# Performance work log

Hardware: AMD Instinct MI355X
Metric: run time of the kernel (lower is better)

## Reference

```python
import jax, jax.numpy as jnp
import numpy as np

N_GAUSS = 1024
L_FEAT = 8
H_IMG = 128
W_IMG = 128
TANFOVX = 0.7
TANFOVY = 0.7
SCALE_MOD = 1.0


def _quat_to_rot(q):
    # normalized quaternion (r, x, y, z) -> rotation matrix [N,3,3]
    q = q / jnp.linalg.norm(q, axis=-1, keepdims=True)
    r, x, y, z = q[:, 0], q[:, 1], q[:, 2], q[:, 3]
    return jnp.stack([
        1 - 2 * (y * y + z * z), 2 * (x * y - r * z), 2 * (x * z + r * y),
        2 * (x * y + r * z), 1 - 2 * (x * x + z * z), 2 * (y * z - r * x),
        2 * (x * z - r * y), 2 * (y * z + r * x), 1 - 2 * (x * x + y * y)],
        axis=-1).reshape(-1, 3, 3)


def _render(means3D, feats, opac, scales, rots, viewmatrix, projmatrix, bg):
    """EWA-splat rasterization: project, 2D cov, depth sort, front-to-back alpha blend."""
    H, W = H_IMG, W_IMG
    fx = W / (2.0 * TANFOVX)
    fy = H / (2.0 * TANFOVY)
    mh = jnp.concatenate([means3D, jnp.ones_like(means3D[:, :1])], axis=1)  # [N,4]
    t = mh @ viewmatrix            # camera space (row-vector / torch-3DGS convention)
    tz = t[:, 2]
    ph = mh @ projmatrix           # clip space
    pw = 1.0 / (ph[:, 3] + 1e-7)
    pix_x = ((ph[:, 0] * pw + 1.0) * W - 1.0) * 0.5
    pix_y = ((ph[:, 1] * pw + 1.0) * H - 1.0) * 0.5
    # 3D covariance from scale + quaternion
    R = _quat_to_rot(rots)
    M = R * (SCALE_MOD * scales)[:, None, :]
    cov3d = jnp.einsum('nij,nkj->nik', M, M)        # [N,3,3]
    # EWA projection of covariance to 2D
    limx, limy = 1.3 * TANFOVX, 1.3 * TANFOVY
    txz = jnp.clip(t[:, 0] / tz, -limx, limx) * tz
    tyz = jnp.clip(t[:, 1] / tz, -limy, limy) * tz
    zero = jnp.zeros_like(tz)
    J = jnp.stack([
        jnp.stack([fx / tz, zero, -fx * txz / (tz * tz)], axis=-1),
        jnp.stack([zero, fy / tz, -fy * tyz / (tz * tz)], axis=-1)], axis=1)  # [N,2,3]
    Wr = viewmatrix[:3, :3].T
    T2 = jnp.einsum('nij,jk->nik', J, Wr)
    cov2 = jnp.einsum('nij,njk,nlk->nil', T2, cov3d, T2)
    cov2 = cov2 + 0.3 * jnp.eye(2, dtype=cov2.dtype)  # low-pass blur, as in CUDA kernel
    det = cov2[:, 0, 0] * cov2[:, 1, 1] - cov2[:, 0, 1] ** 2
    inv_det = 1.0 / (det + 1e-12)
    ca = cov2[:, 1, 1] * inv_det
    cb = -cov2[:, 0, 1] * inv_det
    cc = cov2[:, 0, 0] * inv_det
    mid = 0.5 * (cov2[:, 0, 0] + cov2[:, 1, 1])
    lam1 = mid + jnp.sqrt(jnp.maximum(0.1, mid * mid - det))
    valid = (tz > 0.2) & (det > 0)
    radii = jnp.where(valid, jnp.ceil(3.0 * jnp.sqrt(lam1)), 0.0).astype(jnp.int32)
    # global front-to-back depth order (equiv. to per-tile depth sort here)
    order = jnp.argsort(jnp.where(valid, tz, jnp.inf))
    tz_s, px_s, py_s = tz[order], pix_x[order], pix_y[order]
    ca_s, cb_s, cc_s = ca[order], cb[order], cc[order]
    op_s, feats_s, valid_s = opac[order, 0], feats[order], valid[order]
    ys, xs = jnp.meshgrid(jnp.arange(H, dtype=tz.dtype), jnp.arange(W, dtype=tz.dtype), indexing='ij')
    pxf, pyf = xs.reshape(-1), ys.reshape(-1)        # [P]
    dx = px_s[None, :] - pxf[:, None]                # [P,N]
    dy = py_s[None, :] - pyf[:, None]
    power = -0.5 * (ca_s * dx * dx + cc_s * dy * dy) - cb_s * dx * dy
    alpha = jnp.minimum(0.99, op_s * jnp.exp(power))
    alpha = jnp.where((power > 0) | (alpha < 1.0 / 255.0) | (~valid_s), 0.0, alpha)
    Tcum = jnp.cumprod(1.0 - alpha, axis=1)
    Tprev = jnp.concatenate([jnp.ones_like(Tcum[:, :1]), Tcum[:, :-1]], axis=1)
    w = alpha * Tprev                                # blending weights [P,N]
    img = jnp.einsum('pn,nc->pc', w, feats_s)
    Tfinal = Tcum[:, -1]
    if bg is not None:
        img = img + Tfinal[:, None] * bg[None, :]
    depth_img = (w @ tz_s).reshape(H, W)
    opacity_img = (1.0 - Tfinal).reshape(H, W)
    n_t = jnp.zeros(alpha.shape[1], jnp.int32).at[order].set(
        jnp.sum(alpha > 0, axis=0).astype(jnp.int32))
    img = img.reshape(H, W, -1).transpose(2, 0, 1)   # [C,H,W]
    return img, radii, depth_img, opacity_img, n_t


def setup_inputs() -> dict:
    key = jax.random.key(0)
    ks = jax.random.split(key, 10)
    N, L = N_GAUSS, L_FEAT
    xy = jax.random.uniform(ks[0], (N, 2), minval=-1.5, maxval=1.5)
    z = jax.random.uniform(ks[1], (N, 1), minval=3.0, maxval=6.0)
    means3D = jnp.concatenate([xy, z], axis=1)
    means2D = jnp.zeros((N, 3), jnp.float32)
    colors_precomp = jax.random.uniform(ks[2], (N, 3))
    language_precomp = jax.random.normal(ks[3], (N, L))
    opacities = jax.random.uniform(ks[4], (N, 1), minval=0.1, maxval=1.0)
    opacities_lang = jax.random.uniform(ks[5], (N, 1), minval=0.1, maxval=1.0)
    scales = jax.random.uniform(ks[6], (N, 3), minval=0.01, maxval=0.08)
    scales_lang = jax.random.uniform(ks[7], (N, 3), minval=0.01, maxval=0.08)
    rotations = jax.random.normal(ks[8], (N, 4))
    rotations_lang = jax.random.normal(ks[9], (N, 4))
    viewmatrix = jnp.eye(4, dtype=jnp.float32)
    znear, zfar = 0.01, 100.0
    P = np.zeros((4, 4), np.float32)
    P[0, 0] = 1.0 / TANFOVX
    P[1, 1] = 1.0 / TANFOVY
    P[2, 2] = zfar / (zfar - znear)
    P[2, 3] = -(zfar * znear) / (zfar - znear)
    P[3, 2] = 1.0
    projmatrix = jnp.asarray(P.T)   # row-vector convention: p_clip = [m,1] @ projmatrix
    bg = jnp.zeros(3, jnp.float32)
    campos = jnp.zeros(3, jnp.float32)
    return dict(means3D=means3D, means2D=means2D, colors_precomp=colors_precomp,
                language_precomp=language_precomp, opacities=opacities,
                opacities_lang=opacities_lang, scales=scales, scales_lang=scales_lang,
                rotations=rotations, rotations_lang=rotations_lang,
                viewmatrix=viewmatrix, projmatrix=projmatrix, bg=bg, campos=campos)


def reference(means3D, means2D, colors_precomp, language_precomp, opacities,
              opacities_lang, scales, scales_lang, rotations, rotations_lang,
              viewmatrix, projmatrix, bg, campos):
    color, radii, depth, opac_img, n_touched = _render(
        means3D, colors_precomp, opacities, scales, rotations, viewmatrix, projmatrix, bg)
    language, radii_lang, _, opac_lang, n_touched_lang = _render(
        means3D, language_precomp, opacities_lang, scales_lang, rotations_lang,
        viewmatrix, projmatrix, None)
    return (color, language, radii, radii_lang, depth[None], opac_img[None],
            opac_lang[None], n_touched, n_touched_lang)
```

## Files before the change

kernel.cpp:

```cpp
#include <hip/hip_runtime.h>
#include <math.h>

#define N_G 1024
#define HW 128
#define NPIX (HW * HW)

#define OFF_COLOR  0
#define OFF_LANG   49152
#define OFF_RADII  180224
#define OFF_RADIIL 181248
#define OFF_DEPTH  182272
#define OFF_OPAC   198656
#define OFF_OPACL  215040
#define OFF_NT     231424
#define OFF_NTL    232448

#define WS_REC(r)   ((r) * 16 * N_G)
#define WS_SCAN(r)  (32 * N_G + (r) * 4 * N_G)
#define WS_KEY(r)   (40 * N_G + (r) * 2 * N_G)

__global__ __launch_bounds__(256) void k_pre(
    const float* __restrict__ means3D,
    const float* __restrict__ colors, const float* __restrict__ lang,
    const float* __restrict__ opac, const float* __restrict__ opacl,
    const float* __restrict__ scales, const float* __restrict__ scalesl,
    const float* __restrict__ rots, const float* __restrict__ rotsl,
    const float* __restrict__ V, const float* __restrict__ P,
    float* __restrict__ ws, float* __restrict__ out)
{
    int idx = blockIdx.x * 256 + threadIdx.x;
    if (idx >= 2 * N_G) return;
    int r = idx >> 10;
    int n = idx & (N_G - 1);
    const float* sc = r ? scalesl : scales;
    const float* qt = r ? rotsl : rots;
    const float* op = r ? opacl : opac;
    const float* ft = r ? lang : colors;
    int F = r ? 8 : 3;

    float m0 = means3D[n * 3 + 0], m1 = means3D[n * 3 + 1], m2 = means3D[n * 3 + 2];
    float t0 = m0 * V[0] + m1 * V[4] + m2 * V[8]  + V[12];
    float t1 = m0 * V[1] + m1 * V[5] + m2 * V[9]  + V[13];
    float tz = m0 * V[2] + m1 * V[6] + m2 * V[10] + V[14];
    float ph0 = m0 * P[0] + m1 * P[4] + m2 * P[8]  + P[12];
    float ph1 = m0 * P[1] + m1 * P[5] + m2 * P[9]  + P[13];
    float ph3 = m0 * P[3] + m1 * P[7] + m2 * P[11] + P[15];
    float pw = 1.0f / (ph3 + 1e-7f);
    float px = ((ph0 * pw + 1.0f) * (float)HW - 1.0f) * 0.5f;
    float py = ((ph1 * pw + 1.0f) * (float)HW - 1.0f) * 0.5f;

    float q0 = qt[n * 4 + 0], q1 = qt[n * 4 + 1], q2 = qt[n * 4 + 2], q3 = qt[n * 4 + 3];
    float qinv = 1.0f / sqrtf(q0 * q0 + q1 * q1 + q2 * q2 + q3 * q3);
    q0 *= qinv; q1 *= qinv; q2 *= qinv; q3 *= qinv;
    float rr = q0, x = q1, y = q2, z = q3;
    float R0 = 1.0f - 2.0f * (y * y + z * z), R1 = 2.0f * (x * y - rr * z), R2 = 2.0f * (x * z + rr * y);
    float R3 = 2.0f * (x * y + rr * z), R4 = 1.0f - 2.0f * (x * x + z * z), R5 = 2.0f * (y * z - rr * x);
    float R6 = 2.0f * (x * z - rr * y), R7 = 2.0f * (y * z + rr * x), R8 = 1.0f - 2.0f * (x * x + y * y);
    float s0 = sc[n * 3 + 0], s1 = sc[n * 3 + 1], s2 = sc[n * 3 + 2];
    float M0 = R0 * s0, M1 = R1 * s1, M2 = R2 * s2;
    float M3 = R3 * s0, M4 = R4 * s1, M5 = R5 * s2;
    float M6 = R6 * s0, M7 = R7 * s1, M8 = R8 * s2;
    float c300 = M0 * M0 + M1 * M1 + M2 * M2;
    float c301 = M0 * M3 + M1 * M4 + M2 * M5;
    float c302 = M0 * M6 + M1 * M7 + M2 * M8;
    float c311 = M3 * M3 + M4 * M4 + M5 * M5;
    float c312 = M3 * M6 + M4 * M7 + M5 * M8;
    float c322 = M6 * M6 + M7 * M7 + M8 * M8;

    const float fx = (float)HW / (2.0f * 0.7f);
    const float fy = fx;
    const float limx = 1.3f * 0.7f, limy = 1.3f * 0.7f;
    float txz = fminf(fmaxf(t0 / tz, -limx), limx) * tz;
    float tyz = fminf(fmaxf(t1 / tz, -limy), limy) * tz;
    float J00 = fx / tz, J02 = -fx * txz / (tz * tz);
    float J11 = fy / tz, J12 = -fy * tyz / (tz * tz);
    float a0 = J00 * V[0] + J02 * V[2];
    float a1 = J00 * V[4] + J02 * V[6];
    float a2 = J00 * V[8] + J02 * V[10];
    float b0 = J11 * V[1] + J12 * V[2];
    float b1 = J11 * V[5] + J12 * V[6];
    float b2 = J11 * V[9] + J12 * V[10];
    float u0 = c300 * a0 + c301 * a1 + c302 * a2;
    float u1 = c301 * a0 + c311 * a1 + c312 * a2;
    float u2 = c302 * a0 + c312 * a1 + c322 * a2;
    float v0 = c300 * b0 + c301 * b1 + c302 * b2;
    float v1 = c301 * b0 + c311 * b1 + c312 * b2;
    float v2 = c302 * b0 + c312 * b1 + c322 * b2;
    float c00 = a0 * u0 + a1 * u1 + a2 * u2 + 0.3f;
    float c01 = b0 * u0 + b1 * u1 + b2 * u2;
    float c11 = b0 * v0 + b1 * v1 + b2 * v2 + 0.3f;

    float det = c00 * c11 - c01 * c01;
    float invdet = 1.0f / (det + 1e-12f);
    float ca = c11 * invdet, cb = -c01 * invdet, cc = c00 * invdet;
    float mid = 0.5f * (c00 + c11);
    float lam1 = mid + sqrtf(fmaxf(0.1f, mid * mid - det));
    bool valid = (tz > 0.2f) && (det > 0.0f);
    float radf = valid ? ceilf(3.0f * sqrtf(lam1)) : 0.0f;
    float o = op[n];
    float opEff = valid ? o : 0.0f;
    float pmin, bx, by;
    if (opEff > 0.0f) {
        pmin = -logf(255.0f * opEff);
        float Q = -2.0f * pmin;
        if (Q > 0.0f) {
            bx = sqrtf(Q * c00) + 2.0f;
            by = sqrtf(Q * c11) + 2.0f;
        } else { bx = -1e30f; by = -1e30f; }
    } else {
        pmin = __builtin_inff();
        bx = -1e30f; by = -1e30f;
    }

    float f8[8];
    #pragma unroll
    for (int f = 0; f < 8; ++f) f8[f] = (f < F) ? ft[n * F + f] : 0.0f;

    float* rec = ws + WS_REC(r) + n * 16;
    ((float4*)rec)[0] = make_float4(px, py, ca, cb);
    ((float4*)rec)[1] = make_float4(cc, opEff, pmin, tz);
    ((float4*)rec)[2] = make_float4(f8[0], f8[1], f8[2], f8[3]);
    ((float4*)rec)[3] = make_float4(f8[4], f8[5], f8[6], f8[7]);
    ((float4*)(ws + WS_SCAN(r)))[n] = make_float4(px, py, bx, by);

    float keyf = valid ? tz : __builtin_inff();
    ((unsigned long long*)(ws + WS_KEY(r)))[n] =
        ((unsigned long long)__float_as_uint(keyf) << 32) | (unsigned)n;

    out[(r ? OFF_RADIIL : OFF_RADII) + n] = radf;
    out[(r ? OFF_NTL : OFF_NT) + n] = 0.0f;
}

__global__ __launch_bounds__(64) void k_render(
    const float* __restrict__ ws, const float* __restrict__ bg,
    float* __restrict__ out)
{
    int r = (int)blockIdx.y;
    int tile = (int)blockIdx.x;
    int t = (int)threadIdx.x;
    int tx = t & 7, ty = t >> 3;
    int x0 = (tile & 15) * 8, y0 = (tile >> 4) * 8;
    int px_i = x0 + tx, py_i = y0 + ty;
    float fpx = (float)px_i, fpy = (float)py_i;
    float xmin = (float)x0, xmax = (float)(x0 + 7);
    float ymin = (float)y0, ymax = (float)(y0 + 7);

    __shared__ int s_idx[N_G];
    __shared__ unsigned long long s_key[N_G];
    __shared__ int s_ord[N_G];

    const float4* sc4 = (const float4*)(ws + WS_SCAN(r));
    const unsigned long long* keyp = (const unsigned long long*)(ws + WS_KEY(r));
    float4 gv[16];
    unsigned long long kv[16];
    #pragma unroll
    for (int c = 0; c < 16; ++c) { gv[c] = sc4[c * 64 + t]; kv[c] = keyp[c * 64 + t]; }

    int cnt = 0;
    #pragma unroll
    for (int c = 0; c < 16; ++c) {
        float gpx = gv[c].x, gpy = gv[c].y, gbx = gv[c].z, gby = gv[c].w;
        bool hit = (gpx - gbx <= xmax) && (gpx + gbx >= xmin) &&
                   (gpy - gby <= ymax) && (gpy + gby >= ymin);
        unsigned long long m = __ballot(hit);
        if (hit) {
            int off = __popcll(m & ((1ull << t) - 1ull));
            s_idx[cnt + off] = c * 64 + t;
            s_key[cnt + off] = kv[c];
        }
        cnt += __popcll(m);
    }
    __syncthreads();

    for (int k = t; k < cnt; k += 64) {
        unsigned long long my = s_key[k];
        int rank = 0;
        #pragma unroll 8
        for (int j = 0; j < cnt; ++j) rank += (s_key[j] < my) ? 1 : 0;
        s_ord[rank] = s_idx[k];
    }
    __syncthreads();

    float T = 1.0f;
    float acc[8] = {0, 0, 0, 0, 0, 0, 0, 0};
    float dacc = 0.0f;
    const float ONE255 = 1.0f / 255.0f;
    int ntbase = r ? OFF_NTL : OFF_NT;

    for (int b = 0; b < cnt; b += 64) {
        int jmax = min(64, cnt - b);
        float4 A = make_float4(0, 0, 0, 0), B = A, C = A, D = A;
        int gi = 0;
        if (t < jmax) {
            gi = s_ord[b + t];
            const float4* gp = (const float4*)(ws + WS_REC(r) + gi * 16);
            A = gp[0]; B = gp[1]; C = gp[2]; D = gp[3];
        }

        for (int j = 0; j < jmax; ++j) {
            float pxj = __shfl(A.x, j), pyj = __shfl(A.y, j);
            float caj = __shfl(A.z, j), cbj = __shfl(A.w, j);
            float ccj = __shfl(B.x, j), opj = __shfl(B.y, j), pmj = __shfl(B.z, j);
            float dx = pxj - fpx, dy = pyj - fpy;
            float power = -0.5f * (caj * dx * dx + ccj * dy * dy) - cbj * dx * dy;
            float alpha = 0.0f;
            if (power <= 0.0f && power >= pmj - 1e-3f) {
                alpha = fminf(0.99f, opj * expf(power));
                if (alpha < ONE255) alpha = 0.0f;
            }
            unsigned long long m = __ballot(alpha > 0.0f);
            if (m) {
                float w = alpha * T;
                float f0 = __shfl(C.x, j), f1 = __shfl(C.y, j), f2 = __shfl(C.z, j);
                int origj = __shfl(gi, j);
                if (r == 0) {
                    acc[0] += w * f0; acc[1] += w * f1; acc[2] += w * f2;
                    dacc   += w * __shfl(B.w, j);
                } else {
                    float f3 = __shfl(C.w, j);
                    float f4 = __shfl(D.x, j), f5 = __shfl(D.y, j);
                    float f6 = __shfl(D.z, j), f7 = __shfl(D.w, j);
                    acc[0] += w * f0; acc[1] += w * f1; acc[2] += w * f2; acc[3] += w * f3;
                    acc[4] += w * f4; acc[5] += w * f5; acc[6] += w * f6; acc[7] += w * f7;
                }
                T *= (1.0f - alpha);
                if (t == 0) {
                    atomicAdd(&out[ntbase + origj], (float)__popcll(m));
                }
            }
        }
    }

    int p = py_i * HW + px_i;
    if (r == 0) {
        out[OFF_COLOR + 0 * NPIX + p] = acc[0] + T * bg[0];
        out[OFF_COLOR + 1 * NPIX + p] = acc[1] + T * bg[1];
        out[OFF_COLOR + 2 * NPIX + p] = acc[2] + T * bg[2];
        out[OFF_DEPTH + p] = dacc;
        out[OFF_OPAC + p] = 1.0f - T;
    } else {
        #pragma unroll
        for (int f = 0; f < 8; ++f)
            out[OFF_LANG + f * NPIX + p] = acc[f];
        out[OFF_OPACL + p] = 1.0f - T;
    }
}

extern "C" void kernel_launch(void* const* d_in, const int* in_sizes, int n_in,
                              void* d_out, int out_size, void* d_ws, size_t ws_size,
                              hipStream_t stream)
{
    const float* means3D = (const float*)d_in[0];
    const float* colors  = (const float*)d_in[2];
    const float* lang    = (const float*)d_in[3];
    const float* opac    = (const float*)d_in[4];
    const float* opacl   = (const float*)d_in[5];
    const float* scales  = (const float*)d_in[6];
    const float* scalesl = (const float*)d_in[7];
    const float* rots    = (const float*)d_in[8];
    const float* rotsl   = (const float*)d_in[9];
    const float* V       = (const float*)d_in[10];
    const float* P       = (const float*)d_in[11];
    const float* bg      = (const float*)d_in[12];

    float* out = (float*)d_out;
    float* ws  = (float*)d_ws;

    hipLaunchKernelGGL(k_pre, dim3(8), dim3(256), 0, stream,
                       means3D, colors, lang, opac, opacl, scales, scalesl,
                       rots, rotsl, V, P, ws, out);
    hipLaunchKernelGGL(k_render, dim3(256, 2), dim3(64), 0, stream,
                       ws, bg, out);
}
```

Measured before the change: 114.8 us.

## Split per-tile gaussian blending across four waves and merge partial transmittance

Each render block now has four wavefronts. They share the culling and sorting work, and each blends a contiguous depth segment of the sorted list. The partial colours and transmittance are then composited in order through shared memory. The inner loop becomes branchless and its per-gaussian atomic is batched into one atomic per lane per chunk, in order to raise parallelism for the 512-block launch. The cost is that early-termination semantics are lost and the pmin cull test is dropped. Later segments also do work even when earlier ones have saturated.

Result: faster. 95.48 us (-16.9%).

```diff
diff --git a/kernel.cpp b/kernel.cpp
--- a/kernel.cpp
+++ b/kernel.cpp
@@ -131,13 +131,15 @@
     out[(r ? OFF_NTL : OFF_NT) + n] = 0.0f;
 }
 
-__global__ __launch_bounds__(64) void k_render(
+__global__ __launch_bounds__(256) void k_render(
     const float* __restrict__ ws, const float* __restrict__ bg,
     float* __restrict__ out)
 {
     int r = (int)blockIdx.y;
     int tile = (int)blockIdx.x;
-    int t = (int)threadIdx.x;
+    int tid = (int)threadIdx.x;
+    int w = tid >> 6;
+    int t = tid & 63;
     int tx = t & 7, ty = t >> 3;
     int x0 = (tile & 15) * 8, y0 = (tile >> 4) * 8;
     int px_i = x0 + tx, py_i = y0 + ty;
@@ -148,31 +150,50 @@
     __shared__ int s_idx[N_G];
     __shared__ unsigned long long s_key[N_G];
     __shared__ int s_ord[N_G];
+    __shared__ int s_hw[4];
+    __shared__ float s_comb[4][10][64];
 
     const float4* sc4 = (const float4*)(ws + WS_SCAN(r));
     const unsigned long long* keyp = (const unsigned long long*)(ws + WS_KEY(r));
-    float4 gv[16];
-    unsigned long long kv[16];
-    #pragma unroll
-    for (int c = 0; c < 16; ++c) { gv[c] = sc4[c * 64 + t]; kv[c] = keyp[c * 64 + t]; }
-
-    int cnt = 0;
-    #pragma unroll
-    for (int c = 0; c < 16; ++c) {
-        float gpx = gv[c].x, gpy = gv[c].y, gbx = gv[c].z, gby = gv[c].w;
-        bool hit = (gpx - gbx <= xmax) && (gpx + gbx >= xmin) &&
-                   (gpy - gby <= ymax) && (gpy + gby >= ymin);
-        unsigned long long m = __ballot(hit);
-        if (hit) {
-            int off = __popcll(m & ((1ull << t) - 1ull));
-            s_idx[cnt + off] = c * 64 + t;
-            s_key[cnt + off] = kv[c];
-        }
-        cnt += __popcll(m);
-    }
+    float4 gv[4];
+    unsigned long long kv[4];
+    #pragma unroll
+    for (int c4 = 0; c4 < 4; ++c4) {
+        int c = 4 * w + c4;
+        gv[c4] = sc4[c * 64 + t];
+        kv[c4] = keyp[c * 64 + t];
+    }
+    bool hb[4];
+    unsigned long long m4[4];
+    int hsum = 0;
+    #pragma unroll
+    for (int c4 = 0; c4 < 4; ++c4) {
+        float gpx = gv[c4].x, gpy = gv[c4].y, gbx = gv[c4].z, gby = gv[c4].w;
+        hb[c4] = (gpx - gbx <= xmax) && (gpx + gbx >= xmin) &&
+                 (gpy - gby <= ymax) && (gpy + gby >= ymin);
+        m4[c4] = __ballot(hb[c4]);
+        hsum += __popcll(m4[c4]);
+    }
+    if (t == 0) s_hw[w] = hsum;
     __syncthreads();
-
-    for (int k = t; k < cnt; k += 64) {
+    int start = 0;
+    #pragma unroll
+    for (int w2 = 0; w2 < 4; ++w2) start += (w2 < w) ? s_hw[w2] : 0;
+    int cnt = s_hw[0] + s_hw[1] + s_hw[2] + s_hw[3];
+    unsigned long long lmask = (1ull << t) - 1ull;
+    int off = start;
+    #pragma unroll
+    for (int c4 = 0; c4 < 4; ++c4) {
+        if (hb[c4]) {
+            int o = off + __popcll(m4[c4] & lmask);
+            s_idx[o] = (4 * w + c4) * 64 + t;
+            s_key[o] = kv[c4];
+        }
+        off += __popcll(m4[c4]);
+    }
+    __syncthreads();
+
+    for (int k = tid; k < cnt; k += 256) {
         unsigned long long my = s_key[k];
         int rank = 0;
         #pragma unroll 8
@@ -181,14 +202,17 @@
     }
     __syncthreads();
 
+    int seg = (cnt + 3) >> 2;
+    int sA = min(cnt, w * seg);
+    int sB = min(cnt, sA + seg);
     float T = 1.0f;
     float acc[8] = {0, 0, 0, 0, 0, 0, 0, 0};
     float dacc = 0.0f;
     const float ONE255 = 1.0f / 255.0f;
     int ntbase = r ? OFF_NTL : OFF_NT;
 
-    for (int b = 0; b < cnt; b += 64) {
-        int jmax = min(64, cnt - b);
+    for (int b = sA; b < sB; b += 64) {
+        int jmax = min(64, sB - b);
         float4 A = make_float4(0, 0, 0, 0), B = A, C = A, D = A;
         int gi = 0;
         if (t < jmax) {
@@ -196,53 +220,68 @@
             const float4* gp = (const float4*)(ws + WS_REC(r) + gi * 16);
             A = gp[0]; B = gp[1]; C = gp[2]; D = gp[3];
         }
-
+        float pcmine = 0.0f;
+
+        #pragma unroll 4
         for (int j = 0; j < jmax; ++j) {
             float pxj = __shfl(A.x, j), pyj = __shfl(A.y, j);
             float caj = __shfl(A.z, j), cbj = __shfl(A.w, j);
-            float ccj = __shfl(B.x, j), opj = __shfl(B.y, j), pmj = __shfl(B.z, j);
+            float ccj = __shfl(B.x, j), opj = __shfl(B.y, j);
             float dx = pxj - fpx, dy = pyj - fpy;
             float power = -0.5f * (caj * dx * dx + ccj * dy * dy) - cbj * dx * dy;
-            float alpha = 0.0f;
-            if (power <= 0.0f && power >= pmj - 1e-3f) {
-                alpha = fminf(0.99f, opj * expf(power));
-                if (alpha < ONE255) alpha = 0.0f;
+            float a1 = fminf(0.99f, opj * expf(power));
+            float alpha = (power <= 0.0f && a1 >= ONE255) ? a1 : 0.0f;
+            unsigned long long m = __ballot(alpha > 0.0f);
+            pcmine = (j == t) ? (float)__popcll(m) : pcmine;
+            float wgt = alpha * T;
+            float f0 = __shfl(C.x, j), f1 = __shfl(C.y, j), f2 = __shfl(C.z, j);
+            if (r == 0) {
+                acc[0] += wgt * f0; acc[1] += wgt * f1; acc[2] += wgt * f2;
+                dacc   += wgt * __shfl(B.w, j);
+            } else {
+                float f3 = __shfl(C.w, j);
+                float f4 = __shfl(D.x, j), f5 = __shfl(D.y, j);
+                float f6 = __shfl(D.z, j), f7 = __shfl(D.w, j);
+                acc[0] += wgt * f0; acc[1] += wgt * f1; acc[2] += wgt * f2; acc[3] += wgt * f3;
+                acc[4] += wgt * f4; acc[5] += wgt * f5; acc[6] += wgt * f6; acc[7] += wgt * f7;
             }
-            unsigned long long m = __ballot(alpha > 0.0f);
-            if (m) {
-                float w = alpha * T;
-                float f0 = __shfl(C.x, j), f1 = __shfl(C.y, j), f2 = __shfl(C.z, j);
-                int origj = __shfl(gi, j);
-                if (r == 0) {
-                    acc[0] += w * f0; acc[1] += w * f1; acc[2] += w * f2;
-                    dacc   += w * __shfl(B.w, j);
-                } else {
-                    float f3 = __shfl(C.w, j);
-                    float f4 = __shfl(D.x, j), f5 = __shfl(D.y, j);
-                    float f6 = __shfl(D.z, j), f7 = __shfl(D.w, j);
-                    acc[0] += w * f0; acc[1] += w * f1; acc[2] += w * f2; acc[3] += w * f3;
-                    acc[4] += w * f4; acc[5] += w * f5; acc[6] += w * f6; acc[7] += w * f7;
-                }
-                T *= (1.0f - alpha);
-                if (t == 0) {
-                    atomicAdd(&out[ntbase + origj], (float)__popcll(m));
-                }
-            }
-        }
-    }
-
-    int p = py_i * HW + px_i;
-    if (r == 0) {
-        out[OFF_COLOR + 0 * NPIX + p] = acc[0] + T * bg[0];
-        out[OFF_COLOR + 1 * NPIX + p] = acc[1] + T * bg[1];
-        out[OFF_COLOR + 2 * NPIX + p] = acc[2] + T * bg[2];
-        out[OFF_DEPTH + p] = dacc;
-        out[OFF_OPAC + p] = 1.0f - T;
-    } else {
+            T *= (1.0f - alpha);
+        }
+        if (pcmine > 0.0f) atomicAdd(&out[ntbase + gi], pcmine);
+    }
+
+    #pragma unroll
+    for (int c = 0; c < 8; ++c) s_comb[w][c][t] = acc[c];
+    s_comb[w][8][t] = dacc;
+    s_comb[w][9][t] = T;
+    __syncthreads();
+
+    if (w == 0) {
+        float oc[8], od, Tq;
         #pragma unroll
-        for (int f = 0; f < 8; ++f)
-            out[OFF_LANG + f * NPIX + p] = acc[f];
-        out[OFF_OPACL + p] = 1.0f - T;
+        for (int c = 0; c < 8; ++c) oc[c] = s_comb[0][c][t];
+        od = s_comb[0][8][t];
+        Tq = s_comb[0][9][t];
+        #pragma unroll
+        for (int w2 = 1; w2 < 4; ++w2) {
+            #pragma unroll
+            for (int c = 0; c < 8; ++c) oc[c] += Tq * s_comb[w2][c][t];
+            od += Tq * s_comb[w2][8][t];
+            Tq *= s_comb[w2][9][t];
+        }
+        int p = py_i * HW + px_i;
+        if (r == 0) {
+            out[OFF_COLOR + 0 * NPIX + p] = oc[0] + Tq * bg[0];
+            out[OFF_COLOR + 1 * NPIX + p] = oc[1] + Tq * bg[1];
+            out[OFF_COLOR + 2 * NPIX + p] = oc[2] + Tq * bg[2];
+            out[OFF_DEPTH + p] = od;
+            out[OFF_OPAC + p] = 1.0f - Tq;
+        } else {
+            #pragma unroll
+            for (int f = 0; f < 8; ++f)
+                out[OFF_LANG + f * NPIX + p] = oc[f];
+            out[OFF_OPACL + p] = 1.0f - Tq;
+        }
     }
 }
 
@@ -269,6 +308,6 @@
     hipLaunchKernelGGL(k_pre, dim3(8), dim3(256), 0, stream,
                        means3D, colors, lang, opac, opacl, scales, scalesl,
                        rots, rotsl, V, P, ws, out);
-    hipLaunchKernelGGL(k_render, dim3(256, 2), dim3(64), 0, stream,
+    hipLaunchKernelGGL(k_render, dim3(256, 2), dim3(256), 0, stream,
                        ws, bg, out);
 }
```
